# Performance work log

Measured on AMD Instinct MI355X. Metric: run time of the kernel, lower is better.

## Reference

```python
import jax, jax.numpy as jnp
import numpy as np

RADIUS = 0.1
NSAMPLE = 32


def setup_inputs() -> dict:
    key = jax.random.key(0)
    k1, k2, k3 = jax.random.split(key, 3)
    B, N, P, C = 2, 16384, 4096, 64
    xyz = jax.random.uniform(k1, (B, N, 3), dtype=jnp.float32)
    new_xyz = jax.random.uniform(k2, (B, P, 3), dtype=jnp.float32)
    features = jax.random.normal(k3, (B, C, N), dtype=jnp.float32)
    return {"xyz": xyz, "new_xyz": new_xyz, "features": features}


def _ball_query(xyz, new_xyz, radius, nsample):
    """Return (B, npoint, nsample) int32 indices of the first `nsample` points
    (in original order) within `radius` of each query center. Slots beyond the
    number of valid neighbors are padded with the first valid index (0 if none),
    matching the standard PointNet++ CUDA ball_query semantics."""
    N = xyz.shape[1]
    # squared distances [B, P, N]
    d2 = jnp.sum((new_xyz[:, :, None, :] - xyz[:, None, :, :]) ** 2, axis=-1)
    in_ball = d2 < (radius * radius)
    # score = point index if in ball, else N (sentinel); smallest nsample scores
    # are the first nsample in-ball indices in original order.
    score = jnp.where(in_ball, jnp.arange(N, dtype=jnp.int32), jnp.int32(N))
    neg_topk, _ = jax.lax.top_k(-score, nsample)  # largest of -score == smallest score
    idx = -neg_topk  # [B, P, nsample], ascending
    first = idx[..., :1]
    idx = jnp.where(idx >= N, first, idx)  # pad invalid slots with first valid
    idx = jnp.where(idx >= N, 0, idx)      # no neighbor at all -> 0
    return idx


def _group(features, idx):
    """features (B, C, N), idx (B, P, S) -> (B, C, P, S)"""
    return jax.vmap(lambda f, i: f[:, i])(features, idx)


def reference(xyz, new_xyz, features):
    idx = _ball_query(xyz, new_xyz, RADIUS, NSAMPLE)          # (B, P, S)
    xyz_t = jnp.transpose(xyz, (0, 2, 1))                      # (B, 3, N)
    grouped_xyz = _group(xyz_t, idx)                           # (B, 3, P, S)
    grouped_xyz = grouped_xyz - jnp.transpose(new_xyz, (0, 2, 1))[..., None]
    grouped_features = _group(features, idx)                   # (B, C, P, S)
    new_features = jnp.concatenate([grouped_xyz, grouped_features], axis=1)
    return new_features
```

## Files before the change

kernel.cpp:

```cpp
#include <hip/hip_runtime.h>
#include <limits.h>

#define BB 2
#define NN 16384
#define PP 4096
#define CC 64
#define SS 32
#define R2 0.01f
#define OUTCH (3 + CC)
#define GRES 10
#define NCELL 1000

__device__ __forceinline__ int cell_of(float v) {
  int q = (int)(v * 10.0f);
  return q < 0 ? 0 : (q > GRES - 1 ? GRES - 1 : q);
}
__device__ __forceinline__ int cell_clamp_floor(float v) {
  int q = (int)floorf(v * 10.0f);
  return q < 0 ? 0 : (q > GRES - 1 ? GRES - 1 : q);
}

__global__ __launch_bounds__(1024) void bin_kernel(
    const float* __restrict__ xyz, int* __restrict__ cellStartG,
    float4* __restrict__ sorted4) {
  __shared__ int hist[NCELL];
  __shared__ int fill[NCELL];
  __shared__ int cstart[NCELL];
  __shared__ int wtot[16];
  const int b = blockIdx.x;
  const int t = threadIdx.x;
  const int lane = t & 63;
  const int w = t >> 6;

  if (t < NCELL) { hist[t] = 0; fill[t] = 0; }
  __syncthreads();

  const float* __restrict__ xb = xyz + (size_t)b * NN * 3;
  int cells[16];
#pragma unroll
  for (int k = 0; k < 16; ++k) {
    const int i = t + k * 1024;
    const float x = xb[i * 3 + 0];
    const float y = xb[i * 3 + 1];
    const float z = xb[i * 3 + 2];
    const int c = (cell_of(z) * GRES + cell_of(y)) * GRES + cell_of(x);
    cells[k] = c;
    atomicAdd(&hist[c], 1);
  }
  __syncthreads();

  const int own = (t < NCELL) ? hist[t] : 0;
  int incl = own;
#pragma unroll
  for (int d = 1; d < 64; d <<= 1) {
    const int v = __shfl_up(incl, d);
    if (lane >= d) incl += v;
  }
  if (lane == 63) wtot[w] = incl;
  __syncthreads();
  int pre = 0;
#pragma unroll
  for (int k = 0; k < 16; ++k) pre += (k < w) ? wtot[k] : 0;
  const int excl = pre + incl - own;
  if (t < NCELL) {
    cstart[t] = excl;
    cellStartG[b * 1001 + t] = excl;
  }
  if (t == 0) cellStartG[b * 1001 + NCELL] = NN;
  __syncthreads();

#pragma unroll
  for (int k = 0; k < 16; ++k) {
    const int i = t + k * 1024;
    const float x = xb[i * 3 + 0];
    const float y = xb[i * 3 + 1];
    const float z = xb[i * 3 + 2];
    const int c = cells[k];
    const int r = atomicAdd(&fill[c], 1);
    float4 v;
    v.x = x; v.y = y; v.z = z; v.w = __int_as_float(i);
    sorted4[(size_t)b * NN + cstart[c] + r] = v;
  }
}

__global__ __launch_bounds__(256) void ball_query_grid(
    const float4* __restrict__ sorted4, const int* __restrict__ cellStart,
    const float* __restrict__ new_xyz, int* __restrict__ idx_out) {
#pragma clang fp contract(off)
  __shared__ unsigned bmAll[4 * 576];
  const int widx = threadIdx.x >> 6;
  const int lane = threadIdx.x & 63;
  const int wave = blockIdx.x * 4 + widx;
  const int b = wave >> 12;
  unsigned* bm = bmAll + widx * 576;

  const float cx = new_xyz[wave * 3 + 0];
  const float cy = new_xyz[wave * 3 + 1];
  const float cz = new_xyz[wave * 3 + 2];
  const float4* __restrict__ sb = sorted4 + (size_t)b * NN;
  const int* __restrict__ csb = cellStart + b * 1001;
  int* __restrict__ myout = idx_out + wave * SS;

#pragma unroll
  for (int k = 0; k < 9; ++k) bm[k * 64 + lane] = 0;

  const float mg = 0.1f + 1e-5f;
  const int lox = cell_clamp_floor(cx - mg), hix = cell_clamp_floor(cx + mg);
  const int loy = cell_clamp_floor(cy - mg), hiy = cell_clamp_floor(cy + mg);
  const int loz = cell_clamp_floor(cz - mg), hiz = cell_clamp_floor(cz + mg);
  const int nx = hix - lox + 1;
  const int ny = hiy - loy + 1;
  const int nz = hiz - loz + 1;
  const int nr = nz * ny;

  int s_l = 0, len_l = 0;
  if (lane < nr) {
    int zi, yi;
    if (ny == 1) { zi = lane; yi = 0; }
    else if (ny == 2) { zi = lane >> 1; yi = lane & 1; }
    else { zi = (lane * 11) >> 5; yi = lane - zi * 3; }
    const int c0 = ((loz + zi) * GRES + (loy + yi)) * GRES + lox;
    s_l = csb[c0];
    len_l = csb[c0 + nx] - s_l;
  }
  int incl = len_l;
#pragma unroll
  for (int d = 1; d <= 8; d <<= 1) {
    const int v = __shfl_up(incl, d);
    if (lane >= d) incl += v;
  }
  const int T = __shfl(incl, nr - 1);
  const int Lx = incl - len_l;

  int Lk[9], Sk[9];
#pragma unroll
  for (int k = 0; k < 9; ++k) {
    Lk[k] = __shfl(Lx, k);
    Sk[k] = __shfl(s_l, k);
  }

  for (int t0 = 0; t0 < T; t0 += 64) {
    const int g = t0 + lane;
    if (g < T) {
      int L = Lk[0], S = Sk[0];
#pragma unroll
      for (int k = 1; k < 9; ++k) {
        const bool cge = g >= Lk[k];
        L = cge ? Lk[k] : L;
        S = cge ? Sk[k] : S;
      }
      const float4 pt = sb[S + (g - L)];
      const float dx = cx - pt.x;
      const float dy = cy - pt.y;
      const float dz = cz - pt.z;
      const float a = dx * dx + dy * dy;
      const float d2 = a + dz * dz;
      if (d2 < R2) {
        const int orig = __float_as_int(pt.w);
        const int wi = orig >> 5;
        atomicOr(&bm[(wi >> 3) * 9 + (wi & 7)], 1u << (orig & 31));
      }
    }
  }
  __threadfence_block();

  unsigned wv[8];
  int c = 0;
  int fi = INT_MAX;
#pragma unroll
  for (int k = 0; k < 8; ++k) {
    wv[k] = bm[lane * 9 + k];
    c += (int)__popc(wv[k]);
    if (fi == INT_MAX && wv[k])
      fi = lane * 256 + k * 32 + (int)__builtin_ctz(wv[k]);
  }

  int incl2 = c;
#pragma unroll
  for (int d = 1; d < 64; d <<= 1) {
    const int t = __shfl_up(incl2, d);
    if (lane >= d) incl2 += t;
  }
  const int E = incl2 - c;
  const int total = __shfl(incl2, 63);

  const unsigned long long nb = __ballot(c > 0);
  int fc = 0;
  if (nb) fc = __shfl(fi, (int)__builtin_ctzll(nb));

  int s = E;
  if (s < SS) {
#pragma unroll
    for (int k = 0; k < 8; ++k) {
      unsigned ww = wv[k];
      while (ww && s < SS) {
        const int bpos = (int)__builtin_ctz(ww);
        ww &= ww - 1;
        myout[s++] = lane * 256 + k * 32 + bpos;
      }
      if (s >= SS) break;
    }
  }
  for (int s2 = total + lane; s2 < SS; s2 += 64) myout[s2] = fc;
}

__global__ __launch_bounds__(256) void transpose_feat_kernel(
    const float* __restrict__ feat, float* __restrict__ featT) {
  __shared__ float tile[64][65];
  const int n0 = blockIdx.x * 64;
  const int b = blockIdx.y;
  const int jn = threadIdx.x & 63;
  const int g4 = threadIdx.x >> 6;

  const float* fb = feat + (size_t)b * CC * NN;
#pragma unroll
  for (int k = 0; k < 16; ++k) {
    const int c = g4 * 16 + k;
    tile[c][jn] = fb[(size_t)c * NN + n0 + jn];
  }
  __syncthreads();
  float* ft = featT + ((size_t)b * NN + n0) * CC;
#pragma unroll
  for (int k = 0; k < 16; ++k) {
    const int j = g4 * 16 + k;
    ft[(size_t)j * CC + jn] = tile[jn][j];
  }
}

#define TILE 128
__global__ __launch_bounds__(256) void group_kernel_t(
    const float* __restrict__ xyz, const float* __restrict__ new_xyz,
    const float* __restrict__ featT, const int* __restrict__ idx,
    float* __restrict__ out) {
  __shared__ float lds[TILE * 65];
  const int base = blockIdx.x * TILE;
  const int b = base >> 17;
  const int t = threadIdx.x;
  const size_t PS = (size_t)PP * SS;

  const float4* ftb = (const float4*)(featT + (size_t)b * NN * CC);
#pragma unroll
  for (int k = 0; k < 8; ++k) {
    const int u = k * 256 + t;
    const int r = u >> 4;
    const int q = u & 15;
    const int v = idx[base + r];
    const float4 val = ftb[(size_t)v * 16 + q];
    float* dst = &lds[r * 65 + q * 4];
    dst[0] = val.x; dst[1] = val.y; dst[2] = val.z; dst[3] = val.w;
  }
  __syncthreads();

  if (t < TILE) {
    const int g = base + t;
    const int v = idx[g];
    const int p = (g >> 5) & (PP - 1);
    const float* xr = xyz + ((size_t)b * NN + v) * 3;
    const float* cr = new_xyz + (size_t)(b * PP + p) * 3;
    const size_t ob = (size_t)b * OUTCH * PS + ((size_t)g & (PS - 1));
    out[ob + 0 * PS] = xr[0] - cr[0];
    out[ob + 1 * PS] = xr[1] - cr[1];
    out[ob + 2 * PS] = xr[2] - cr[2];
  }

  float* ob3 = out + (size_t)b * OUTCH * PS + 3 * PS + ((size_t)base & (PS - 1));
#pragma unroll
  for (int k = 0; k < 32; ++k) {
    const int u = k * 256 + t;
    const int c = u >> 7;
    const int r = u & 127;
    ob3[(size_t)c * PS + r] = lds[r * 65 + c];
  }
}

extern "C" void kernel_launch(void* const* d_in, const int* in_sizes, int n_in,
                              void* d_out, int out_size, void* d_ws, size_t ws_size,
                              hipStream_t stream) {
  const float* xyz = (const float*)d_in[0];
  const float* new_xyz = (const float*)d_in[1];
  const float* feat = (const float*)d_in[2];
  float* out = (float*)d_out;

  const size_t idxBytes = (size_t)BB * PP * SS * sizeof(int);
  int* idx = (int*)d_ws;
  char* ovl = (char*)d_ws + idxBytes;
  float* featT = (float*)ovl;
  float4* sorted4 = (float4*)ovl;
  int* cellStart = (int*)(ovl + (size_t)BB * NN * sizeof(float4));

  bin_kernel<<<BB, 1024, 0, stream>>>(xyz, cellStart, sorted4);
  ball_query_grid<<<(BB * PP) / 4, 256, 0, stream>>>(sorted4, cellStart, new_xyz, idx);
  transpose_feat_kernel<<<dim3(NN / 64, BB), 256, 0, stream>>>(feat, featT);
  group_kernel_t<<<(BB * PP * SS) / TILE, 256, 0, stream>>>(xyz, new_xyz, featT,
                                                            idx, out);
}
```

Baseline: 63.29 us.

## Fuse ball query with feature grouping, keeping neighbor indices in shared memory

Merges the ball-query kernel and the grouping kernel into one. Each block of four waves computes 128 neighbor indices into shared memory and then gathers and writes the grouped features directly. The global idx buffer round trip and one kernel launch go away, and the bitmap and the gather tile share one LDS buffer. The workspace is laid out so featT and sorted4 no longer overlap. The cost is a heavier fused kernel, and the grouping step now waits on the slowest wave's query through a block barrier.

Measured after the change: 61.06 us. 1.04x faster.

```diff
diff --git a/kernel.cpp b/kernel.cpp
--- a/kernel.cpp
+++ b/kernel.cpp
@@ -10,6 +10,7 @@
 #define OUTCH (3 + CC)
 #define GRES 10
 #define NCELL 1000
+#define TILE 128
 
 __device__ __forceinline__ int cell_of(float v) {
   int q = (int)(v * 10.0f);
@@ -83,23 +84,48 @@
   }
 }
 
-__global__ __launch_bounds__(256) void ball_query_grid(
+__global__ __launch_bounds__(256) void transpose_feat_kernel(
+    const float* __restrict__ feat, float* __restrict__ featT) {
+  __shared__ float tile[64][65];
+  const int n0 = blockIdx.x * 64;
+  const int b = blockIdx.y;
+  const int jn = threadIdx.x & 63;
+  const int g4 = threadIdx.x >> 6;
+
+  const float* fb = feat + (size_t)b * CC * NN;
+#pragma unroll
+  for (int k = 0; k < 16; ++k) {
+    const int c = g4 * 16 + k;
+    tile[c][jn] = fb[(size_t)c * NN + n0 + jn];
+  }
+  __syncthreads();
+  float* ft = featT + ((size_t)b * NN + n0) * CC;
+#pragma unroll
+  for (int k = 0; k < 16; ++k) {
+    const int j = g4 * 16 + k;
+    ft[(size_t)j * CC + jn] = tile[jn][j];
+  }
+}
+
+__global__ __launch_bounds__(256) void query_group_kernel(
     const float4* __restrict__ sorted4, const int* __restrict__ cellStart,
-    const float* __restrict__ new_xyz, int* __restrict__ idx_out) {
+    const float* __restrict__ new_xyz, const float* __restrict__ xyz,
+    const float* __restrict__ featT, float* __restrict__ out) {
 #pragma clang fp contract(off)
-  __shared__ unsigned bmAll[4 * 576];
+  __shared__ float smem[TILE * 65];
+  __shared__ int idxsm[TILE];
   const int widx = threadIdx.x >> 6;
   const int lane = threadIdx.x & 63;
   const int wave = blockIdx.x * 4 + widx;
   const int b = wave >> 12;
-  unsigned* bm = bmAll + widx * 576;
+  unsigned* bm = (unsigned*)smem + widx * 576;
+  int* myout = idxsm + widx * SS;
 
   const float cx = new_xyz[wave * 3 + 0];
   const float cy = new_xyz[wave * 3 + 1];
   const float cz = new_xyz[wave * 3 + 2];
   const float4* __restrict__ sb = sorted4 + (size_t)b * NN;
   const int* __restrict__ csb = cellStart + b * 1001;
-  int* __restrict__ myout = idx_out + wave * SS;
 
 #pragma unroll
   for (int k = 0; k < 9; ++k) bm[k * 64 + lane] = 0;
@@ -202,39 +228,10 @@
     }
   }
   for (int s2 = total + lane; s2 < SS; s2 += 64) myout[s2] = fc;
-}
-
-__global__ __launch_bounds__(256) void transpose_feat_kernel(
-    const float* __restrict__ feat, float* __restrict__ featT) {
-  __shared__ float tile[64][65];
-  const int n0 = blockIdx.x * 64;
-  const int b = blockIdx.y;
-  const int jn = threadIdx.x & 63;
-  const int g4 = threadIdx.x >> 6;
-
-  const float* fb = feat + (size_t)b * CC * NN;
-#pragma unroll
-  for (int k = 0; k < 16; ++k) {
-    const int c = g4 * 16 + k;
-    tile[c][jn] = fb[(size_t)c * NN + n0 + jn];
-  }
-  __syncthreads();
-  float* ft = featT + ((size_t)b * NN + n0) * CC;
-#pragma unroll
-  for (int k = 0; k < 16; ++k) {
-    const int j = g4 * 16 + k;
-    ft[(size_t)j * CC + jn] = tile[jn][j];
-  }
-}
-
-#define TILE 128
-__global__ __launch_bounds__(256) void group_kernel_t(
-    const float* __restrict__ xyz, const float* __restrict__ new_xyz,
-    const float* __restrict__ featT, const int* __restrict__ idx,
-    float* __restrict__ out) {
-  __shared__ float lds[TILE * 65];
+
+  __syncthreads();
+
   const int base = blockIdx.x * TILE;
-  const int b = base >> 17;
   const int t = threadIdx.x;
   const size_t PS = (size_t)PP * SS;
 
@@ -244,16 +241,16 @@
     const int u = k * 256 + t;
     const int r = u >> 4;
     const int q = u & 15;
-    const int v = idx[base + r];
+    const int v = idxsm[r];
     const float4 val = ftb[(size_t)v * 16 + q];
-    float* dst = &lds[r * 65 + q * 4];
+    float* dst = &smem[r * 65 + q * 4];
     dst[0] = val.x; dst[1] = val.y; dst[2] = val.z; dst[3] = val.w;
   }
   __syncthreads();
 
   if (t < TILE) {
     const int g = base + t;
-    const int v = idx[g];
+    const int v = idxsm[t];
     const int p = (g >> 5) & (PP - 1);
     const float* xr = xyz + ((size_t)b * NN + v) * 3;
     const float* cr = new_xyz + (size_t)(b * PP + p) * 3;
@@ -267,9 +264,9 @@
 #pragma unroll
   for (int k = 0; k < 32; ++k) {
     const int u = k * 256 + t;
-    const int c = u >> 7;
+    const int c2 = u >> 7;
     const int r = u & 127;
-    ob3[(size_t)c * PS + r] = lds[r * 65 + c];
+    ob3[(size_t)c2 * PS + r] = smem[r * 65 + c2];
   }
 }
 
@@ -281,16 +278,13 @@
   const float* feat = (const float*)d_in[2];
   float* out = (float*)d_out;
 
-  const size_t idxBytes = (size_t)BB * PP * SS * sizeof(int);
-  int* idx = (int*)d_ws;
-  char* ovl = (char*)d_ws + idxBytes;
-  float* featT = (float*)ovl;
-  float4* sorted4 = (float4*)ovl;
-  int* cellStart = (int*)(ovl + (size_t)BB * NN * sizeof(float4));
+  float* featT = (float*)d_ws;
+  const size_t featTBytes = (size_t)BB * NN * CC * sizeof(float);
+  float4* sorted4 = (float4*)((char*)d_ws + featTBytes);
+  int* cellStart = (int*)((char*)d_ws + featTBytes + (size_t)BB * NN * sizeof(float4));
 
   bin_kernel<<<BB, 1024, 0, stream>>>(xyz, cellStart, sorted4);
-  ball_query_grid<<<(BB * PP) / 4, 256, 0, stream>>>(sorted4, cellStart, new_xyz, idx);
   transpose_feat_kernel<<<dim3(NN / 64, BB), 256, 0, stream>>>(feat, featT);
-  group_kernel_t<<<(BB * PP * SS) / TILE, 256, 0, stream>>>(xyz, new_xyz, featT,
-                                                            idx, out);
-}
+  query_group_kernel<<<(BB * PP) / 4, 256, 0, stream>>>(sorted4, cellStart,
+                                                        new_xyz, xyz, featT, out);
+}
```
